# Kernel optimization log

Measured on AMD Instinct MI355X. Metric: run time of the kernel, lower is better.

## Reference

```python
import jax, jax.numpy as jnp
import numpy as np

N_KNOTS = 32


def _safe_dist(a, b):
    # a: (B, P, 3), b: (B, M, 3) -> (B, P, M) euclidean distance,
    # with zero (not NaN) gradient at coincident points (diagonal of K_train).
    diff = a[:, :, None, :] - b[:, None, :, :]
    sq = jnp.sum(diff * diff, axis=-1)
    safe = jnp.where(sq > 0, sq, 1.0)
    return jnp.where(sq > 0, jnp.sqrt(safe), 0.0)


def setup_inputs() -> dict:
    key = jax.random.key(0)
    k1, k2 = jax.random.split(key)
    B = 8
    raw = jax.random.uniform(k1, (B, 3, 448, 448), dtype=jnp.float32)
    params_tensor = jax.random.uniform(k2, (B, 6 * N_KNOTS + 3), dtype=jnp.float32)
    return {"raw": raw, "params_tensor": params_tensor}


def reference(raw, params_tensor):
    n = N_KNOTS
    B, C, H, W = raw.shape
    dt = raw.dtype
    # get_params
    xs = params_tensor[:, : 3 * n].reshape(B, n, 3)
    ys = params_tensor[:, 3 * n : 6 * n].reshape(B, n, 3)
    lambdas = params_tensor[:, 6 * n :].reshape(B, 3)
    # NOTE: original code does raw.reshape(B, H*W, C) (NOT a permute) -- replicate exactly.
    fimg = raw.reshape(B, H * W, C)
    # build_k: K_pred (B, HW, n+4)
    d_pred = _safe_dist(fimg, xs)
    K_pred = jnp.concatenate([d_pred, jnp.ones((B, H * W, 1), dt), fimg], axis=2)
    # shared pieces of build_k_train
    dd = _safe_dist(xs, xs)                      # (B, n, n)
    eye = jnp.eye(n, dtype=dt)
    ones_top = jnp.ones((B, n, 1), dt)
    bottom_left = jnp.concatenate([jnp.ones((B, 1, n), dt), jnp.transpose(xs, (0, 2, 1))], axis=1)
    bottom = jnp.concatenate([bottom_left, jnp.zeros((B, 4, 4), dt)], axis=2)  # (B, 4, n+4)
    zs = jnp.zeros((B, 4, 1), dt)
    ws = []
    for i in range(3):  # fixed small channel loop
        d_l = dd + lambdas[:, i][:, None, None] * eye
        top = jnp.concatenate([d_l, ones_top, xs], axis=2)        # (B, n, n+4)
        K = jnp.concatenate([top, bottom], axis=1)                # (B, n+4, n+4)
        v = jnp.concatenate([ys[:, :, i : i + 1], zs], axis=1)    # (B, n+4, 1)
        ws.append(jnp.linalg.pinv(K) @ v)
    Wmat = jnp.concatenate(ws, axis=2)            # (B, n+4, 3)
    out = K_pred @ Wmat                            # (B, HW, 3)
    return out.reshape(raw.shape)
```

## Files before the change

kernel.cpp:

```cpp
#include <hip/hip_runtime.h>
#include <math.h>

#define NK 32
#define NP 36
#define PX 16

typedef float v2f __attribute__((ext_vector_type(2)));

__device__ __forceinline__ float hw_sqrtf(float x) {
    return __builtin_amdgcn_sqrtf(x);
}

__device__ __forceinline__ float bcastf(float v, int sl) {
    return __int_as_float(__builtin_amdgcn_readlane(__float_as_int(v), sl));
}

__device__ __forceinline__ v2f pks(float s, v2f b, v2f c) {
    return __builtin_elementwise_fma((v2f){s, s}, b, c);
}
__device__ __forceinline__ v2f pkv(v2f a, v2f b, v2f c) {
    return __builtin_elementwise_fma(a, b, c);
}

__device__ __forceinline__ void apply_chunk8(const float4* __restrict__ src,
                                             float4* __restrict__ dst,
                                             const float4* __restrict__ sX,
                                             const float4* __restrict__ sW4,
                                             float4 wb, float4 w33,
                                             float4 w34, float4 w35) {
    float4 v0 = src[0], v1 = src[1], v2 = src[2],
           v3 = src[3], v4 = src[4], v5 = src[5];
    float f[24] = {v0.x, v0.y, v0.z, v0.w, v1.x, v1.y, v1.z, v1.w,
                   v2.x, v2.y, v2.z, v2.w, v3.x, v3.y, v3.z, v3.w,
                   v4.x, v4.y, v4.z, v4.w, v5.x, v5.y, v5.z, v5.w};

    v2f fx[4], fy[4], fz[4], pn[4];
    #pragma unroll
    for (int q = 0; q < 4; ++q) {
        fx[q] = (v2f){f[6*q+0], f[6*q+3]};
        fy[q] = (v2f){f[6*q+1], f[6*q+4]};
        fz[q] = (v2f){f[6*q+2], f[6*q+5]};
        pn[q] = pkv(fz[q], fz[q], pkv(fy[q], fy[q], fx[q] * fx[q]));
    }

    v2f ax[4], ay[4], az[4];
    #pragma unroll
    for (int q = 0; q < 4; ++q) {
        ax[q] = pks(w35.x, fz[q], pks(w34.x, fy[q], pks(w33.x, fx[q], (v2f){wb.x, wb.x})));
        ay[q] = pks(w35.y, fz[q], pks(w34.y, fy[q], pks(w33.y, fx[q], (v2f){wb.y, wb.y})));
        az[q] = pks(w35.z, fz[q], pks(w34.z, fy[q], pks(w33.z, fx[q], (v2f){wb.z, wb.z})));
    }

    #pragma unroll 4
    for (int k = 0; k < NK; ++k) {
        float4 xk = sX[k];
        float4 wk = sW4[k];
        #pragma unroll
        for (int q = 0; q < 4; ++q) {
            v2f t = pn[q] + (v2f){xk.w, xk.w};
            t = pks(xk.x, fx[q], t);
            t = pks(xk.y, fy[q], t);
            t = pks(xk.z, fz[q], t);
            t = __builtin_elementwise_max(t, (v2f){0.f, 0.f});
            v2f d = (v2f){hw_sqrtf(t[0]), hw_sqrtf(t[1])};
            ax[q] = pks(wk.x, d, ax[q]);
            ay[q] = pks(wk.y, d, ay[q]);
            az[q] = pks(wk.z, d, az[q]);
        }
    }

    #pragma unroll
    for (int u = 0; u < 2; ++u) {
        int a = 2*u, c = 2*u + 1;
        dst[3*u+0] = make_float4(ax[a][0], ay[a][0], az[a][0], ax[a][1]);
        dst[3*u+1] = make_float4(ay[a][1], az[a][1], ax[c][0], ay[c][0]);
        dst[3*u+2] = make_float4(az[c][0], ax[c][1], ay[c][1], az[c][1]);
    }
}

__global__ __launch_bounds__(256, 2) void tps_fused(const float* __restrict__ raw,
                                                    const float* __restrict__ params,
                                                    float* __restrict__ out,
                                                    int HW) {
    __shared__ float  sxs[NK * 3];
    __shared__ float4 sX[NK];
    __shared__ float4 sW4[NP];

    int b   = blockIdx.y;
    int tid = threadIdx.x;
    const float* pp = params + (size_t)b * (6 * NK + 3);

    if (tid < NK * 3) sxs[tid] = pp[tid];
    __syncthreads();

    int wid  = tid >> 6;
    int lane = tid & 63;

    if (wid < 3) {
        int ch = wid;
        float lam = pp[6 * NK + ch];

        int li = (lane < NK) ? lane : 0;
        float myx0 = sxs[li*3+0], myx1 = sxs[li*3+1], myx2 = sxs[li*3+2];

        float rr0,rr1,rr2,rr3,rr4,rr5,rr6,rr7,rr8,rr9,rr10,rr11,rr12,rr13,
              rr14,rr15,rr16,rr17,rr18,rr19,rr20,rr21,rr22,rr23,rr24,rr25,
              rr26,rr27,rr28,rr29,rr30,rr31,rr32,rr33,rr34,rr35,rr36;

        float bcomp = (lane == 33) ? 0.f : (lane == 34) ? 1.f : 2.f;
#define BUILDC(c) do {                                                        \
    float xc0 = sxs[(c)*3+0], xc1 = sxs[(c)*3+1], xc2 = sxs[(c)*3+2];         \
    float dx = myx0 - xc0, dy = myx1 - xc1, dz = myx2 - xc2;                  \
    float d  = hw_sqrtf(dx*dx + dy*dy + dz*dz);                               \
    float v;                                                                  \
    if (lane < NK)       v = (lane == (c)) ? lam : d;                         \
    else if (lane == 32) v = 1.0f;                                            \
    else if (lane < NP)  v = (bcomp==0.f)?xc0:(bcomp==1.f)?xc1:xc2;           \
    else                 v = 0.0f;                                            \
    rr##c = v;                                                                \
} while (0)
        BUILDC(0);  BUILDC(1);  BUILDC(2);  BUILDC(3);  BUILDC(4);  BUILDC(5);
        BUILDC(6);  BUILDC(7);  BUILDC(8);  BUILDC(9);  BUILDC(10); BUILDC(11);
        BUILDC(12); BUILDC(13); BUILDC(14); BUILDC(15); BUILDC(16); BUILDC(17);
        BUILDC(18); BUILDC(19); BUILDC(20); BUILDC(21); BUILDC(22); BUILDC(23);
        BUILDC(24); BUILDC(25); BUILDC(26); BUILDC(27); BUILDC(28); BUILDC(29);
        BUILDC(30); BUILDC(31);
#undef BUILDC
        bool top = (lane < NK);
        rr32 = top ? 1.0f : 0.0f;
        rr33 = top ? myx0 : 0.0f;
        rr34 = top ? myx1 : 0.0f;
        rr35 = top ? myx2 : 0.0f;
        rr36 = top ? pp[3*NK + li*3 + ch] : 0.0f;

#define COLU(c) if ((c) > KK) { rr##c -= minv * bcastf(rr##c, KK); }
#define ALLCOLS \
    COLU(1)  COLU(2)  COLU(3)  COLU(4)  COLU(5)  COLU(6)  COLU(7)  COLU(8)  \
    COLU(9)  COLU(10) COLU(11) COLU(12) COLU(13) COLU(14) COLU(15) COLU(16) \
    COLU(17) COLU(18) COLU(19) COLU(20) COLU(21) COLU(22) COLU(23) COLU(24) \
    COLU(25) COLU(26) COLU(27) COLU(28) COLU(29) COLU(30) COLU(31) COLU(32) \
    COLU(33) COLU(34) COLU(35) COLU(36)
#define STEP(Kv) do {                                                         \
    const int KK = (Kv);                                                      \
    float pv  = bcastf(rr##Kv, (Kv));                                         \
    float inv = __builtin_amdgcn_rcpf(pv);                                    \
    bool  isp = (lane == (Kv));                                               \
    float minv = isp ? (1.0f - inv) : rr##Kv * inv;                           \
    ALLCOLS                                                                   \
} while (0)

        STEP(0);  STEP(1);  STEP(2);  STEP(3);  STEP(4);  STEP(5);
        STEP(6);  STEP(7);  STEP(8);  STEP(9);  STEP(10); STEP(11);
        STEP(12); STEP(13); STEP(14); STEP(15); STEP(16); STEP(17);
        STEP(18); STEP(19); STEP(20); STEP(21); STEP(22); STEP(23);
        STEP(24); STEP(25); STEP(26); STEP(27); STEP(28); STEP(29);
        STEP(30); STEP(31); STEP(32); STEP(33); STEP(34); STEP(35);
#undef STEP
#undef ALLCOLS
#undef COLU

        if (lane < NP)
            ((float*)&sW4[lane])[ch] = rr36;
    } else {
        if (lane < NK) {
            float x0 = sxs[lane*3+0], x1 = sxs[lane*3+1], x2 = sxs[lane*3+2];
            sX[lane] = make_float4(-2.f*x0, -2.f*x1, -2.f*x2,
                                   x0*x0 + x1*x1 + x2*x2);
        }
    }
    __syncthreads();

    int p16 = blockIdx.x * 256 + tid;
    size_t base = (size_t)b * HW * 3 + (size_t)p16 * (PX * 3);

    float4 wb  = sW4[NK];
    float4 w33 = sW4[NK+1], w34 = sW4[NK+2], w35 = sW4[NK+3];

    apply_chunk8((const float4*)(raw + base),      (float4*)(out + base),
                 sX, sW4, wb, w33, w34, w35);
    apply_chunk8((const float4*)(raw + base + 24), (float4*)(out + base + 24),
                 sX, sW4, wb, w33, w34, w35);
}

extern "C" void kernel_launch(void* const* d_in, const int* in_sizes, int n_in,
                              void* d_out, int out_size, void* d_ws, size_t ws_size,
                              hipStream_t stream) {
    const float* raw    = (const float*)d_in[0];
    const float* params = (const float*)d_in[1];
    float* out = (float*)d_out;

    int B  = in_sizes[1] / (6 * NK + 3);
    int HW = in_sizes[0] / (B * 3);

    int groups = HW / PX;
    int bpb = (groups + 255) / 256;
    tps_fused<<<dim3(bpb, B), dim3(256), 0, stream>>>(raw, params, out, HW);
}
```

Baseline: 32.57 us.

## Solve TPS system once per batch and share via grid sync

```diff
diff --git a/kernel.cpp b/kernel.cpp
--- a/kernel.cpp
+++ b/kernel.cpp
@@ -1,9 +1,11 @@
 #include <hip/hip_runtime.h>
+#include <hip/hip_cooperative_groups.h>
 #include <math.h>
 
 #define NK 32
 #define NP 36
 #define PX 16
+#define WSN 68
 
 typedef float v2f __attribute__((ext_vector_type(2)));
 
@@ -78,10 +80,11 @@
     }
 }
 
-__global__ __launch_bounds__(256, 2) void tps_fused(const float* __restrict__ raw,
-                                                    const float* __restrict__ params,
-                                                    float* __restrict__ out,
-                                                    int HW) {
+__global__ __launch_bounds__(256, 2) void tps_coop(const float* __restrict__ raw,
+                                                   const float* __restrict__ params,
+                                                   float* __restrict__ out,
+                                                   float4* __restrict__ ws,
+                                                   int HW) {
     __shared__ float  sxs[NK * 3];
     __shared__ float4 sX[NK];
     __shared__ float4 sW4[NP];
@@ -89,25 +92,28 @@
     int b   = blockIdx.y;
     int tid = threadIdx.x;
     const float* pp = params + (size_t)b * (6 * NK + 3);
-
-    if (tid < NK * 3) sxs[tid] = pp[tid];
-    __syncthreads();
-
-    int wid  = tid >> 6;
-    int lane = tid & 63;
-
-    if (wid < 3) {
-        int ch = wid;
-        float lam = pp[6 * NK + ch];
-
-        int li = (lane < NK) ? lane : 0;
-        float myx0 = sxs[li*3+0], myx1 = sxs[li*3+1], myx2 = sxs[li*3+2];
-
-        float rr0,rr1,rr2,rr3,rr4,rr5,rr6,rr7,rr8,rr9,rr10,rr11,rr12,rr13,
-              rr14,rr15,rr16,rr17,rr18,rr19,rr20,rr21,rr22,rr23,rr24,rr25,
-              rr26,rr27,rr28,rr29,rr30,rr31,rr32,rr33,rr34,rr35,rr36;
-
-        float bcomp = (lane == 33) ? 0.f : (lane == 34) ? 1.f : 2.f;
+    float4* wsb = ws + (size_t)b * WSN;
+
+    if (blockIdx.x == 0) {
+        if (tid < NK * 3) sxs[tid] = pp[tid];
+        __syncthreads();
+
+        int wid  = tid >> 6;
+        int lane = tid & 63;
+
+        if (wid < 3) {
+            int ch = wid;
+            float lam = pp[6 * NK + ch];
+
+            int li = (lane < NK) ? lane : 0;
+            float myx0 = sxs[li*3+0], myx1 = sxs[li*3+1], myx2 = sxs[li*3+2];
+
+            float rr0,rr1,rr2,rr3,rr4,rr5,rr6,rr7,rr8,rr9,rr10,rr11,rr12,
+                  rr13,rr14,rr15,rr16,rr17,rr18,rr19,rr20,rr21,rr22,rr23,
+                  rr24,rr25,rr26,rr27,rr28,rr29,rr30,rr31,rr32,rr33,rr34,
+                  rr35,rr36;
+
+            float bcomp = (lane == 33) ? 0.f : (lane == 34) ? 1.f : 2.f;
 #define BUILDC(c) do {                                                        \
     float xc0 = sxs[(c)*3+0], xc1 = sxs[(c)*3+1], xc2 = sxs[(c)*3+2];         \
     float dx = myx0 - xc0, dy = myx1 - xc1, dz = myx2 - xc2;                  \
@@ -119,19 +125,20 @@
     else                 v = 0.0f;                                            \
     rr##c = v;                                                                \
 } while (0)
-        BUILDC(0);  BUILDC(1);  BUILDC(2);  BUILDC(3);  BUILDC(4);  BUILDC(5);
-        BUILDC(6);  BUILDC(7);  BUILDC(8);  BUILDC(9);  BUILDC(10); BUILDC(11);
-        BUILDC(12); BUILDC(13); BUILDC(14); BUILDC(15); BUILDC(16); BUILDC(17);
-        BUILDC(18); BUILDC(19); BUILDC(20); BUILDC(21); BUILDC(22); BUILDC(23);
-        BUILDC(24); BUILDC(25); BUILDC(26); BUILDC(27); BUILDC(28); BUILDC(29);
-        BUILDC(30); BUILDC(31);
+            BUILDC(0);  BUILDC(1);  BUILDC(2);  BUILDC(3);  BUILDC(4);
+            BUILDC(5);  BUILDC(6);  BUILDC(7);  BUILDC(8);  BUILDC(9);
+            BUILDC(10); BUILDC(11); BUILDC(12); BUILDC(13); BUILDC(14);
+            BUILDC(15); BUILDC(16); BUILDC(17); BUILDC(18); BUILDC(19);
+            BUILDC(20); BUILDC(21); BUILDC(22); BUILDC(23); BUILDC(24);
+            BUILDC(25); BUILDC(26); BUILDC(27); BUILDC(28); BUILDC(29);
+            BUILDC(30); BUILDC(31);
 #undef BUILDC
-        bool top = (lane < NK);
-        rr32 = top ? 1.0f : 0.0f;
-        rr33 = top ? myx0 : 0.0f;
-        rr34 = top ? myx1 : 0.0f;
-        rr35 = top ? myx2 : 0.0f;
-        rr36 = top ? pp[3*NK + li*3 + ch] : 0.0f;
+            bool top = (lane < NK);
+            rr32 = top ? 1.0f : 0.0f;
+            rr33 = top ? myx0 : 0.0f;
+            rr34 = top ? myx1 : 0.0f;
+            rr35 = top ? myx2 : 0.0f;
+            rr36 = top ? pp[3*NK + li*3 + ch] : 0.0f;
 
 #define COLU(c) if ((c) > KK) { rr##c -= minv * bcastf(rr##c, KK); }
 #define ALLCOLS \
@@ -149,25 +156,31 @@
     ALLCOLS                                                                   \
 } while (0)
 
-        STEP(0);  STEP(1);  STEP(2);  STEP(3);  STEP(4);  STEP(5);
-        STEP(6);  STEP(7);  STEP(8);  STEP(9);  STEP(10); STEP(11);
-        STEP(12); STEP(13); STEP(14); STEP(15); STEP(16); STEP(17);
-        STEP(18); STEP(19); STEP(20); STEP(21); STEP(22); STEP(23);
-        STEP(24); STEP(25); STEP(26); STEP(27); STEP(28); STEP(29);
-        STEP(30); STEP(31); STEP(32); STEP(33); STEP(34); STEP(35);
+            STEP(0);  STEP(1);  STEP(2);  STEP(3);  STEP(4);  STEP(5);
+            STEP(6);  STEP(7);  STEP(8);  STEP(9);  STEP(10); STEP(11);
+            STEP(12); STEP(13); STEP(14); STEP(15); STEP(16); STEP(17);
+            STEP(18); STEP(19); STEP(20); STEP(21); STEP(22); STEP(23);
+            STEP(24); STEP(25); STEP(26); STEP(27); STEP(28); STEP(29);
+            STEP(30); STEP(31); STEP(32); STEP(33); STEP(34); STEP(35);
 #undef STEP
 #undef ALLCOLS
 #undef COLU
 
-        if (lane < NP)
-            ((float*)&sW4[lane])[ch] = rr36;
-    } else {
-        if (lane < NK) {
-            float x0 = sxs[lane*3+0], x1 = sxs[lane*3+1], x2 = sxs[lane*3+2];
-            sX[lane] = make_float4(-2.f*x0, -2.f*x1, -2.f*x2,
-                                   x0*x0 + x1*x1 + x2*x2);
+            if (lane < NP)
+                ((float*)&wsb[lane])[ch] = rr36;
+        } else {
+            if (lane < NK) {
+                float x0 = sxs[lane*3+0], x1 = sxs[lane*3+1], x2 = sxs[lane*3+2];
+                wsb[NP + lane] = make_float4(-2.f*x0, -2.f*x1, -2.f*x2,
+                                             x0*x0 + x1*x1 + x2*x2);
+            }
         }
     }
+
+    cooperative_groups::this_grid().sync();
+
+    if (tid < NP)            sW4[tid]      = wsb[tid];
+    else if (tid < NP + NK)  sX[tid - NP]  = wsb[tid];
     __syncthreads();
 
     int p16 = blockIdx.x * 256 + tid;
@@ -187,12 +200,18 @@
                               hipStream_t stream) {
     const float* raw    = (const float*)d_in[0];
     const float* params = (const float*)d_in[1];
-    float* out = (float*)d_out;
+    float* out  = (float*)d_out;
+    float4* ws  = (float4*)d_ws;
 
     int B  = in_sizes[1] / (6 * NK + 3);
     int HW = in_sizes[0] / (B * 3);
 
     int groups = HW / PX;
     int bpb = (groups + 255) / 256;
-    tps_fused<<<dim3(bpb, B), dim3(256), 0, stream>>>(raw, params, out, HW);
-}
+
+    dim3 grid(bpb, B), block(256);
+    void* args[] = {(void*)&raw, (void*)&params, (void*)&out,
+                    (void*)&ws, (void*)&HW};
+    hipLaunchCooperativeKernel((const void*)tps_coop, grid, block,
+                               args, 0, stream);
+}
```

Result: slower. 72.65 us (+123.1%).
